# Kernel optimization log

Hardware: AMD Instinct MI355X
Metric: run time of the kernel (lower is better)

Reference implementation:

```python
import jax, jax.numpy as jnp
import numpy as np

B, N, L = 2, 2048, 2048
DQ, DKV, H, WF = 1024, 1024, 16, 4
HD = DQ // H
EPS = 1e-5


def _ln(x, g, b):
    m = jnp.mean(x, axis=-1, keepdims=True)
    v = jnp.mean(jnp.square(x - m), axis=-1, keepdims=True)
    return (x - m) * jax.lax.rsqrt(v + EPS) * g + b


def setup_inputs() -> dict:
    key = jax.random.key(0)
    ks = jax.random.split(key, 12)
    s = 0.02
    return {
        "x_q": jax.random.normal(ks[0], (B, N, DQ), jnp.float32),
        "x_kv": jax.random.normal(ks[1], (B, L, DKV), jnp.float32),
        "qn_g": jnp.ones((DQ,), jnp.float32),
        "qn_b": jnp.zeros((DQ,), jnp.float32),
        "kvn_g": jnp.ones((DKV,), jnp.float32),
        "kvn_b": jnp.zeros((DKV,), jnp.float32),
        "Wq": jax.random.normal(ks[2], (DQ, DQ), jnp.float32) * s,
        "bq": jnp.zeros((DQ,), jnp.float32),
        "Wk": jax.random.normal(ks[3], (DQ, DKV), jnp.float32) * s,
        "bk": jnp.zeros((DQ,), jnp.float32),
        "Wv": jax.random.normal(ks[4], (DQ, DKV), jnp.float32) * s,
        "bv": jnp.zeros((DQ,), jnp.float32),
        "Wo": jax.random.normal(ks[5], (DQ, DQ), jnp.float32) * s,
        "bo": jnp.zeros((DQ,), jnp.float32),
        "n2_g": jnp.ones((DQ,), jnp.float32),
        "n2_b": jnp.zeros((DQ,), jnp.float32),
        "W1": jax.random.normal(ks[6], (WF * DQ, DQ), jnp.float32) * s,
        "b1": jnp.zeros((WF * DQ,), jnp.float32),
        "W2": jax.random.normal(ks[7], (DQ, WF * DQ), jnp.float32) * s,
        "b2": jnp.zeros((DQ,), jnp.float32),
    }


def reference(x_q, x_kv, qn_g, qn_b, kvn_g, kvn_b, Wq, bq, Wk, bk, Wv, bv,
              Wo, bo, n2_g, n2_b, W1, b1, W2, b2):
    # projections (torch Linear: x @ W.T + b)
    q = (_ln(x_q, qn_g, qn_b) @ Wq.T + bq).reshape(B, N, H, HD)
    kvn = _ln(x_kv, kvn_g, kvn_b)
    k = (kvn @ Wk.T + bk).reshape(B, L, H, HD)
    v = (kvn @ Wv.T + bv).reshape(B, L, H, HD)

    # attention with softmax-1: exp(s)/(1 + sum exp(s)), numerically stable
    scale = 1.0 / jnp.sqrt(jnp.float32(HD))
    s = jnp.einsum("bnhd,blhd->bhnl", q, k) * scale  # [B,H,N,L]
    m = jnp.max(s, axis=-1, keepdims=True)
    m = jnp.maximum(m, 0.0)  # include the implicit zero logit of softmax-1
    p = jnp.exp(s - m)
    denom = jnp.sum(p, axis=-1, keepdims=True) + jnp.exp(-m)
    attn = p / denom
    attn_out = jnp.einsum("bhnl,blhd->bnhd", attn, v).reshape(B, N, DQ)

    # residual + out proj
    x = x_q + (attn_out @ Wo.T + bo)
    # residual MLP (GELU, exact/erf as torch nn.GELU default)
    h = jax.nn.gelu(_ln(x, n2_g, n2_b) @ W1.T + b1, approximate=False)
    x = x + (h @ W2.T + b2)
    return x
```

## Files before the change

kernel.cpp:

```cpp
#include <hip/hip_runtime.h>
#include <hip/hip_bf16.h>
#include <stdint.h>

#define DEV __device__ __forceinline__

typedef unsigned short ushort_t;
typedef __attribute__((ext_vector_type(8))) short bf16x8;
typedef __attribute__((ext_vector_type(4))) float f32x4;

DEV uint32_t f2bf2(float lo, float hi) {
  uint32_t d;
  asm("v_cvt_pk_bf16_f32 %0, %1, %2" : "=v"(d) : "v"(lo), "v"(hi));
  return d;
}
DEV ushort_t f2bf(float f) { return (ushort_t)f2bf2(f, f); }

DEV void gload_lds16(const void* gp, void* lp) {
  __builtin_amdgcn_global_load_lds(
      (__attribute__((address_space(1))) void*)(void*)(uintptr_t)gp,
      (__attribute__((address_space(3))) void*)lp, 16, 0, 0);
}

DEV float gelu_fast(float x) {
  const float z = fabsf(x) * 0.70710678118654752f;
  const float t = __builtin_amdgcn_rcpf(fmaf(0.3275911f, z, 1.0f));
  float p = fmaf(1.061405429f, t, -1.453152027f);
  p = fmaf(p, t, 1.421413741f);
  p = fmaf(p, t, -0.284496736f);
  p = fmaf(p, t, 0.254829592f);
  p *= t;
  const float e = __builtin_amdgcn_exp2f(z * z * -1.4426950408889634f);
  const float er = fmaf(-p, e, 1.0f);
  const float s = copysignf(er, x);
  return 0.5f * x * (1.0f + s);
}

DEV void ln_row(const float* __restrict__ x, const float* __restrict__ g,
                const float* __restrict__ be, ushort_t* __restrict__ out, int row) {
  const int t = threadIdx.x;
  const float4 v = ((const float4*)(x + (size_t)row * 1024))[t];
  float s = v.x + v.y + v.z + v.w;
  float sq = v.x * v.x + v.y * v.y + v.z * v.z + v.w * v.w;
#pragma unroll
  for (int d = 1; d < 64; d <<= 1) { s += __shfl_xor(s, d); sq += __shfl_xor(sq, d); }
  __shared__ float sm[8];
  const int w = t >> 6, lane = t & 63;
  if (lane == 0) { sm[w * 2] = s; sm[w * 2 + 1] = sq; }
  __syncthreads();
  s = sm[0] + sm[2] + sm[4] + sm[6];
  sq = sm[1] + sm[3] + sm[5] + sm[7];
  const float mean = s * (1.f / 1024.f);
  const float var = sq * (1.f / 1024.f) - mean * mean;
  const float rstd = rsqrtf(var + 1e-5f);
  const float4 gv = ((const float4*)g)[t];
  const float4 bv = ((const float4*)be)[t];
  uint2 o;
  o.x = f2bf2((v.x - mean) * rstd * gv.x + bv.x, (v.y - mean) * rstd * gv.y + bv.y);
  o.y = f2bf2((v.z - mean) * rstd * gv.z + bv.z, (v.w - mean) * rstd * gv.w + bv.w);
  ((uint2*)(out + (size_t)row * 1024))[t] = o;
}

__global__ __launch_bounds__(256) void cvt_ln(
    const float* __restrict__ Wq, const float* __restrict__ Wk,
    const float* __restrict__ Wv, const float* __restrict__ Wo,
    const float* __restrict__ W1, const float* __restrict__ W2,
    ushort_t* __restrict__ WQKVB, ushort_t* __restrict__ WoB,
    ushort_t* __restrict__ W1B, ushort_t* __restrict__ W2B,
    const float* __restrict__ x_q, const float* __restrict__ x_kv,
    const float* __restrict__ qg, const float* __restrict__ qb,
    const float* __restrict__ kg, const float* __restrict__ kb,
    ushort_t* __restrict__ oq, ushort_t* __restrict__ okv) {
  if (blockIdx.x < 12288) {
    int i = blockIdx.x * 256 + threadIdx.x;
    const float* src; ushort_t* dst; int j;
    if (i < 262144)            { src = Wq; dst = WQKVB;            j = i; }
    else if (i < 524288)       { src = Wk; dst = WQKVB + 1048576;  j = i - 262144; }
    else if (i < 786432)       { src = Wv; dst = WQKVB + 2097152;  j = i - 524288; }
    else if (i < 1048576)      { src = Wo; dst = WoB;              j = i - 786432; }
    else if (i < 2097152)      { src = W1; dst = W1B;              j = i - 1048576; }
    else                       { src = W2; dst = W2B;              j = i - 2097152; }
    float4 v = ((const float4*)src)[j];
    uint2 o; o.x = f2bf2(v.x, v.y); o.y = f2bf2(v.z, v.w);
    ((uint2*)dst)[j] = o;
  } else {
    const int r = blockIdx.x - 12288;
    if (r < 4096) ln_row(x_q, qg, qb, oq, r);
    else ln_row(x_kv, kg, kb, okv, r - 4096);
  }
}

__global__ __launch_bounds__(256) void ln_bf16(const float* __restrict__ x,
                                               const float* __restrict__ g,
                                               const float* __restrict__ be,
                                               ushort_t* __restrict__ out) {
  ln_row(x, g, be, out, blockIdx.x);
}

DEV void xcd_remap(int gx, int gy, int& bx, int& by) {
  const int lin = by * gx + bx;
  const int xcd = lin & 7, s = lin >> 3;
  by = xcd * (gy >> 3) + s / gx;
  bx = s % gx;
}

enum { EPI_BF16 = 0, EPI_KV = 1, EPI_RESID = 2, EPI_GELU = 3, EPI_QKV = 4 };

template <int BM, int TN, int BK, int EPI>
__global__ __launch_bounds__(256, (BM == 64) ? 4 : 3) void gemm_bt(
    const ushort_t* __restrict__ A,
    const ushort_t* __restrict__ A2,
    const ushort_t* __restrict__ Wb,
    const float* __restrict__ bias, const float* __restrict__ bias2,
    const float* __restrict__ bias3,
    const float* __restrict__ resid,
    void* __restrict__ outp, void* __restrict__ outp2, void* __restrict__ outp3,
    int M, int N, int K, float oscale) {
  constexpr int WAVES_N = (TN == 128 || BM == 64) ? 2 : 1;
  constexpr int WAVES_M = 4 / WAVES_N;
  constexpr int NI = BM / WAVES_M / 16;
  constexpr int NJ = TN / WAVES_N / 16;
  constexpr int CH = BK / 8;
  constexpr int NA = (BM * CH) / 256;
  constexpr int NBL = (TN * CH) / 256;
  constexpr int KS = BK / 32;
  __shared__ ushort_t As[2][BM * BK];
  __shared__ ushort_t Bs[2][TN * BK];
  const int t = threadIdx.x;
  const int w = t >> 6, lane = t & 63;
  const int qd = lane >> 4, ql = lane & 15;
  int bx = blockIdx.x, by = blockIdx.y;
  xcd_remap(gridDim.x, gridDim.y, bx, by);
  const int m0 = by * BM, n0 = bx * TN;
  const int wm = (w / WAVES_N) * (BM / WAVES_M);
  const int wn = (w % WAVES_N) * (TN / WAVES_N);
  const int sw = (BK == 64) ? (ql & 7) : ((ql >> 1) & 3);

  const ushort_t* Ause = (EPI == EPI_QKV && n0 >= 1024) ? A2 : A;

  const ushort_t* pa[NA];
#pragma unroll
  for (int p = 0; p < NA; p++) {
    int n = p * 256 + t, row = n / CH, c = n % CH;
    int g = (BK == 64) ? (c ^ (row & 7)) : (c ^ ((row >> 1) & 3));
    pa[p] = Ause + (size_t)(m0 + row) * K + g * 8;
  }
  const ushort_t* pb[NBL];
#pragma unroll
  for (int p = 0; p < NBL; p++) {
    int n = p * 256 + t, row = n / CH, c = n % CH;
    int g = (BK == 64) ? (c ^ (row & 7)) : (c ^ ((row >> 1) & 3));
    pb[p] = Wb + (size_t)(n0 + row) * K + g * 8;
  }

#pragma unroll
  for (int p = 0; p < NA; p++) { gload_lds16(pa[p], &As[0][(p * 256 + t) * 8]); pa[p] += BK; }
#pragma unroll
  for (int p = 0; p < NBL; p++) { gload_lds16(pb[p], &Bs[0][(p * 256 + t) * 8]); pb[p] += BK; }
  __syncthreads();

  f32x4 acc[NI][NJ] = {};
  const int NIT = K / BK;
  int cur = 0;

  for (int it = 0; it < NIT; ++it) {
    if (it + 1 < NIT) {
#pragma unroll
      for (int p = 0; p < NA; p++) { gload_lds16(pa[p], &As[1 ^ cur][(p * 256 + t) * 8]); pa[p] += BK; }
#pragma unroll
      for (int p = 0; p < NBL; p++) { gload_lds16(pb[p], &Bs[1 ^ cur][(p * 256 + t) * 8]); pb[p] += BK; }
    }
    const ushort_t* Ac = As[cur];
    const ushort_t* Bc = Bs[cur];
#pragma unroll
    for (int ks = 0; ks < KS; ks++) {
      bf16x8 af[NI], bf[NJ];
#pragma unroll
      for (int i = 0; i < NI; i++)
        af[i] = *(const bf16x8*)&Ac[(wm + i * 16 + ql) * BK + ((ks * 4 + qd) ^ sw) * 8];
#pragma unroll
      for (int j = 0; j < NJ; j++)
        bf[j] = *(const bf16x8*)&Bc[(wn + j * 16 + ql) * BK + ((ks * 4 + qd) ^ sw) * 8];
#pragma unroll
      for (int i = 0; i < NI; i++)
#pragma unroll
        for (int j = 0; j < NJ; j++)
          acc[i][j] = __builtin_amdgcn_mfma_f32_16x16x32_bf16(af[i], bf[j], acc[i][j], 0, 0, 0);
    }
    __syncthreads();
    cur ^= 1;
  }

#pragma unroll
  for (int i = 0; i < NI; i++) {
    const int mr = m0 + wm + i * 16 + qd * 4;
#pragma unroll
    for (int j = 0; j < NJ; j++) {
      const int col = n0 + wn + j * 16 + ql;
      f32x4 v = acc[i][j];
      if constexpr (EPI == EPI_BF16) {
        const float bb = bias[col];
        ushort_t* o = (ushort_t*)outp;
#pragma unroll
        for (int r = 0; r < 4; r++) o[(size_t)(mr + r) * N + col] = f2bf((v[r] + bb) * oscale);
      } else if constexpr (EPI == EPI_QKV) {
        if (col < 1024) {
          const float bb = bias[col];
          ushort_t* o = (ushort_t*)outp;
#pragma unroll
          for (int r = 0; r < 4; r++) o[(size_t)(mr + r) * 1024 + col] = f2bf((v[r] + bb) * oscale);
        } else if (col < 2048) {
          const int c2 = col - 1024;
          const float bb = bias2[c2];
          ushort_t* o = (ushort_t*)outp2;
#pragma unroll
          for (int r = 0; r < 4; r++) o[(size_t)(mr + r) * 1024 + c2] = f2bf(v[r] + bb);
        } else {
          const int vc = col - 2048;
          const float bb = bias3[vc];
          const int h = vc >> 6, d = vc & 63;
          const int b = mr >> 11, l0 = mr & 2047;
          uint2 pk;
          pk.x = f2bf2(v[0] + bb, v[1] + bb);
          pk.y = f2bf2(v[2] + bb, v[3] + bb);
          *(uint2*)((ushort_t*)outp3 + ((((size_t)b * 16 + h) * 64 + d) * 2048 + l0)) = pk;
        }
      } else if constexpr (EPI == EPI_RESID) {
        const float bb = bias[col];
        float* o = (float*)outp;
#pragma unroll
        for (int r = 0; r < 4; r++) {
          size_t idx = (size_t)(mr + r) * N + col;
          o[idx] = resid[idx] + v[r] + bb;
        }
      } else if constexpr (EPI == EPI_GELU) {
        const float bb = bias[col];
        ushort_t* o = (ushort_t*)outp;
#pragma unroll
        for (int r = 0; r < 4; r++)
          o[(size_t)(mr + r) * N + col] = f2bf(gelu_fast(v[r] + bb));
      }
    }
  }
}

template <int EPI>
__global__ __launch_bounds__(512, 2) void gemm256v2(
    const ushort_t* __restrict__ A, const ushort_t* __restrict__ Wb,
    const float* __restrict__ bias,
    void* __restrict__ outp, int M, int N, int K, float oscale) {
  __shared__ ushort_t As[2][256 * 64];
  __shared__ ushort_t Bs[2][256 * 64];
  const int t = threadIdx.x;
  const int w = t >> 6, lane = t & 63;
  const int qd = lane >> 4, ql = lane & 15;
  const int wr = w >> 2, wc = w & 3;
  int bx = blockIdx.x, by = blockIdx.y;
  xcd_remap(gridDim.x, gridDim.y, bx, by);
  const int m0 = by * 256, n0 = bx * 256;
  const int sw = ql & 7;

  const ushort_t* pa[4];
  const ushort_t* pb[4];
#pragma unroll
  for (int p = 0; p < 4; p++) {
    const int n = p * 512 + t, row = n >> 3, c = (n & 7) ^ (row & 7);
    pa[p] = A + (size_t)(m0 + row) * K + c * 8;
    pb[p] = Wb + (size_t)(n0 + row) * K + c * 8;
  }

#pragma unroll
  for (int p = 0; p < 4; p++) { gload_lds16(pa[p], &As[0][(p * 512 + t) * 8]); pa[p] += 64; }
#pragma unroll
  for (int p = 0; p < 4; p++) { gload_lds16(pb[p], &Bs[0][(p * 512 + t) * 8]); pb[p] += 64; }
  __syncthreads();

  f32x4 acc[8][4] = {};
  const int NT = K / 64;
  int cur = 0;

#define AFREAD(KS)                                                              \
  _Pragma("unroll") for (int i = 0; i < 8; i++)                                 \
      af[i] = *(const bf16x8*)&Ac[(wr * 128 + i * 16 + ql) * 64 +               \
                                  (((KS) * 4 + qd) ^ sw) * 8];
#define BFREAD(KS, NH)                                                          \
  _Pragma("unroll") for (int jj = 0; jj < 2; jj++)                              \
      bf[jj] = *(const bf16x8*)&Bc[(wc * 64 + (NH) * 32 + jj * 16 + ql) * 64 +  \
                                   (((KS) * 4 + qd) ^ sw) * 8];
#define MM(NH)                                                                  \
  __builtin_amdgcn_s_setprio(1);                                                \
  _Pragma("unroll") for (int i = 0; i < 8; i++)                                 \
      _Pragma("unroll") for (int jj = 0; jj < 2; jj++)                          \
          acc[i][(NH) * 2 + jj] = __builtin_amdgcn_mfma_f32_16x16x32_bf16(      \
              af[i], bf[jj], acc[i][(NH) * 2 + jj], 0, 0, 0);                   \
  __builtin_amdgcn_s_setprio(0);

  for (int T = 0; T < NT; ++T) {
    const ushort_t* Ac = As[cur];
    const ushort_t* Bc = Bs[cur];
    ushort_t* An = As[cur ^ 1];
    ushort_t* Bn = Bs[cur ^ 1];
    const bool st = (T + 1 < NT);
    bf16x8 af[8], bf[2];

    if (st) {
#pragma unroll
      for (int p = 0; p < 4; p++) { gload_lds16(pa[p], &An[(p * 512 + t) * 8]); pa[p] += 64; }
#pragma unroll
      for (int p = 0; p < 4; p++) { gload_lds16(pb[p], &Bn[(p * 512 + t) * 8]); pb[p] += 64; }
    }
    AFREAD(0)
    BFREAD(0, 0)
    MM(0)
    __builtin_amdgcn_s_barrier();

    BFREAD(0, 1)
    MM(1)
    __builtin_amdgcn_s_barrier();

    AFREAD(1)
    BFREAD(1, 0)
    MM(0)
    __builtin_amdgcn_s_barrier();

    BFREAD(1, 1)
    MM(1)
    if (st) asm volatile("s_waitcnt vmcnt(0)" ::: "memory");
    __builtin_amdgcn_sched_barrier(0);
    __builtin_amdgcn_s_barrier();
    __builtin_amdgcn_sched_barrier(0);
    cur ^= 1;
  }
#undef AFREAD
#undef BFREAD
#undef MM

#pragma unroll
  for (int i = 0; i < 8; i++) {
    const int mr = m0 + wr * 128 + i * 16 + qd * 4;
#pragma unroll
    for (int j = 0; j < 4; j++) {
      const int col = n0 + wc * 64 + j * 16 + ql;
      f32x4 v = acc[i][j];
      if constexpr (EPI == EPI_GELU) {
        const float bb = bias[col];
        ushort_t* o = (ushort_t*)outp;
#pragma unroll
        for (int r = 0; r < 4; r++)
          o[(size_t)(mr + r) * N + col] = f2bf(gelu_fast(v[r] + bb));
      } else if constexpr (EPI == EPI_BF16) {
        const float bb = bias[col];
        ushort_t* o = (ushort_t*)outp;
#pragma unroll
        for (int r = 0; r < 4; r++)
          o[(size_t)(mr + r) * N + col] = f2bf((v[r] + bb) * oscale);
      }
    }
  }
}

__global__ __launch_bounds__(256, 2) void flash_attn(const ushort_t* __restrict__ Qg,
                                                     const ushort_t* __restrict__ Kg,
                                                     const ushort_t* __restrict__ VTg,
                                                     ushort_t* __restrict__ Og) {
  __shared__ ushort_t QPs[128 * 64];
  __shared__ ushort_t Ks[2][64 * 64];
  __shared__ ushort_t Vs[2][64 * 64];
  const int t = threadIdx.x, w = t >> 6, lane = t & 63;
  const int qd = lane >> 4, ql = lane & 15;
  int bx = blockIdx.x, bh = blockIdx.y;
  xcd_remap(gridDim.x, gridDim.y, bx, bh);
  const int b = bh >> 4, h = bh & 15;
  const int n0 = bx * 128;
  const ushort_t* Qp = Qg + ((size_t)b * 2048 + n0) * 1024 + h * 64;
  const ushort_t* Kp = Kg + (size_t)b * 2048 * 1024 + h * 64;
  const ushort_t* Vp = VTg + (size_t)bh * 64 * 2048;
  const int sw = ql & 7;

  const ushort_t* kp2[2];
  const ushort_t* vp2[2];
#pragma unroll
  for (int p = 0; p < 2; p++) {
    int n = p * 256 + t, row = n >> 3, c = (n & 7) ^ (row & 7);
    kp2[p] = Kp + (size_t)row * 1024 + c * 8;
    vp2[p] = Vp + (size_t)row * 2048 + c * 8;
  }

#pragma unroll
  for (int p = 0; p < 4; p++) {
    int n = p * 256 + t, row = n >> 3, c = (n & 7) ^ (row & 7);
    gload_lds16(Qp + (size_t)row * 1024 + c * 8, &QPs[n * 8]);
  }
#pragma unroll
  for (int p = 0; p < 2; p++) {
    int n = p * 256 + t;
    gload_lds16(kp2[p], &Ks[0][n * 8]);
    gload_lds16(vp2[p], &Vs[0][n * 8]);
    kp2[p] += 64 * 1024;
    vp2[p] += 64;
  }
  __syncthreads();

  bf16x8 aq[2][2];
#pragma unroll
  for (int i = 0; i < 2; i++)
#pragma unroll
    for (int ks = 0; ks < 2; ks++)
      aq[i][ks] = *(const bf16x8*)&QPs[(w * 32 + i * 16 + ql) * 64 + ((ks * 4 + qd) ^ sw) * 8];
  __syncthreads();

  f32x4 accO[2][4] = {};
  float lro2[2] = {0.f, 0.f};

  int cur = 0;
  for (int lt = 0; lt < 32; ++lt) {
    if (lt + 1 < 32) {
#pragma unroll
      for (int p = 0; p < 2; p++) {
        int n = p * 256 + t;
        gload_lds16(kp2[p], &Ks[1 ^ cur][n * 8]);
        gload_lds16(vp2[p], &Vs[1 ^ cur][n * 8]);
        kp2[p] += 64 * 1024;
        vp2[p] += 64;
      }
    }
    const ushort_t* Kc = Ks[cur];
    const ushort_t* Vc = Vs[cur];

    f32x4 accS[4][2] = {};
#pragma unroll
    for (int ks = 0; ks < 2; ks++) {
      bf16x8 bk[4];
#pragma unroll
      for (int j = 0; j < 4; j++)
        bk[j] = *(const bf16x8*)&Kc[(j * 16 + ql) * 64 + ((ks * 4 + qd) ^ sw) * 8];
      __builtin_amdgcn_s_setprio(1);
#pragma unroll
      for (int j = 0; j < 4; j++)
#pragma unroll
        for (int i = 0; i < 2; i++)
          accS[j][i] = __builtin_amdgcn_mfma_f32_16x16x32_bf16(bk[j], aq[i][ks], accS[j][i], 0, 0, 0);
      __builtin_amdgcn_s_setprio(0);
    }

#pragma unroll
    for (int j = 0; j < 4; j++)
#pragma unroll
      for (int i = 0; i < 2; i++) {
        f32x4 p;
#pragma unroll
        for (int r = 0; r < 4; r++) {
          p[r] = __builtin_amdgcn_exp2f(accS[j][i][r]);
          lro2[i] += p[r];
        }
        const int n = w * 32 + i * 16 + ql;
        const int coff = (((j * 2 + (qd >> 1)) ^ sw) << 3) + ((qd & 1) << 2);
        uint2 pk; pk.x = f2bf2(p[0], p[1]); pk.y = f2bf2(p[2], p[3]);
        *(uint2*)&QPs[n * 64 + coff] = pk;
      }

#pragma unroll
    for (int ks = 0; ks < 2; ks++) {
      bf16x8 ap[2], bv[4];
#pragma unroll
      for (int i = 0; i < 2; i++)
        ap[i] = *(const bf16x8*)&QPs[(w * 32 + i * 16 + ql) * 64 + ((ks * 4 + qd) ^ sw) * 8];
#pragma unroll
      for (int jo = 0; jo < 4; jo++)
        bv[jo] = *(const bf16x8*)&Vc[(jo * 16 + ql) * 64 + ((ks * 4 + qd) ^ sw) * 8];
      __builtin_amdgcn_s_setprio(1);
#pragma unroll
      for (int i = 0; i < 2; i++)
#pragma unroll
        for (int jo = 0; jo < 4; jo++)
          accO[i][jo] = __builtin_amdgcn_mfma_f32_16x16x32_bf16(ap[i], bv[jo], accO[i][jo], 0, 0, 0);
      __builtin_amdgcn_s_setprio(0);
    }

    __syncthreads();
    cur ^= 1;
  }

  float dn[2];
#pragma unroll
  for (int i = 0; i < 2; i++) {
    float l = lro2[i];
    l += __shfl_xor(l, 16);
    l += __shfl_xor(l, 32);
    dn[i] = l + 1.0f;
  }

#pragma unroll
  for (int i = 0; i < 2; i++)
#pragma unroll
    for (int r = 0; r < 4; r++) {
      const float inv = 1.0f / __shfl(dn[i], qd * 4 + r);
      const int row = n0 + w * 32 + i * 16 + qd * 4 + r;
#pragma unroll
      for (int jo = 0; jo < 4; jo++)
        Og[((size_t)b * 2048 + row) * 1024 + h * 64 + jo * 16 + ql] =
            f2bf(accO[i][jo][r] * inv);
    }
}

extern "C" void kernel_launch(void* const* d_in, const int* in_sizes, int n_in,
                              void* d_out, int out_size, void* d_ws, size_t ws_size,
                              hipStream_t stream) {
  const float* x_q = (const float*)d_in[0];
  const float* x_kv = (const float*)d_in[1];
  const float* qn_g = (const float*)d_in[2];
  const float* qn_b = (const float*)d_in[3];
  const float* kvn_g = (const float*)d_in[4];
  const float* kvn_b = (const float*)d_in[5];
  const float* Wq = (const float*)d_in[6];
  const float* bq = (const float*)d_in[7];
  const float* Wk = (const float*)d_in[8];
  const float* bk = (const float*)d_in[9];
  const float* Wv = (const float*)d_in[10];
  const float* bv = (const float*)d_in[11];
  const float* Wo = (const float*)d_in[12];
  const float* bo = (const float*)d_in[13];
  const float* n2_g = (const float*)d_in[14];
  const float* n2_b = (const float*)d_in[15];
  const float* W1 = (const float*)d_in[16];
  const float* b1 = (const float*)d_in[17];
  const float* W2 = (const float*)d_in[18];
  const float* b2 = (const float*)d_in[19];

  char* ws = (char*)d_ws;
  const size_t MB = 1ull << 20;
  ushort_t* WQKVB = (ushort_t*)(ws + 0 * MB);
  ushort_t* WoB = (ushort_t*)(ws + 6 * MB);
  ushort_t* W1B = (ushort_t*)(ws + 8 * MB);
  ushort_t* W2B = (ushort_t*)(ws + 16 * MB);
  ushort_t* LNQ = (ushort_t*)(ws + 24 * MB);
  ushort_t* LNKV = (ushort_t*)(ws + 32 * MB);
  ushort_t* Qb = (ushort_t*)(ws + 40 * MB);
  ushort_t* Kb = (ushort_t*)(ws + 48 * MB);
  ushort_t* VTb = (ushort_t*)(ws + 56 * MB);
  ushort_t* AOb = (ushort_t*)(ws + 64 * MB);
  float* Xf = (float*)(ws + 72 * MB);
  ushort_t* LN2 = (ushort_t*)(ws + 88 * MB);
  ushort_t* Hb = (ushort_t*)(ws + 24 * MB);

  const float QSCALE = 0.18033688011112042f;

  cvt_ln<<<20480, 256, 0, stream>>>(Wq, Wk, Wv, Wo, W1, W2, WQKVB, WoB, W1B, W2B,
                                    x_q, x_kv, qn_g, qn_b, kvn_g, kvn_b, LNQ, LNKV);

  gemm_bt<128, 128, 32, EPI_QKV><<<dim3(24, 32), 256, 0, stream>>>(
      LNQ, LNKV, WQKVB, bq, bk, bv, nullptr, Qb, Kb, VTb, 4096, 3072, 1024, QSCALE);

  flash_attn<<<dim3(16, 32), 256, 0, stream>>>(Qb, Kb, VTb, AOb);

  gemm_bt<64, 64, 64, EPI_RESID><<<dim3(16, 64), 256, 0, stream>>>(
      AOb, nullptr, WoB, bo, nullptr, nullptr, x_q, Xf, nullptr, nullptr,
      4096, 1024, 1024, 1.0f);
  ln_bf16<<<4096, 256, 0, stream>>>(Xf, n2_g, n2_b, LN2);
  gemm256v2<EPI_GELU><<<dim3(16, 16), 512, 0, stream>>>(
      LN2, W1B, b1, Hb, 4096, 4096, 1024, 1.0f);
  gemm_bt<64, 64, 64, EPI_RESID><<<dim3(16, 64), 256, 0, stream>>>(
      Hb, nullptr, W2B, b2, nullptr, nullptr, Xf, (float*)d_out, nullptr, nullptr,
      4096, 1024, 4096, 1.0f);
}
```

Before: 354.3 us.

## Software-pipeline attention loop so next tile's QK overlaps current softmax and PV

Restructures the flash-attention main loop into a two-stage software pipeline. K is staged one tile ahead of V, and the QK^T MFMAs for tile t+1 are issued before the exp2/softmax and PV MFMAs of tile t, using alternating accumulators accA and accB. The aim is to fill the MFMA units during the transcendental and LDS write phases and to hide load latency. The cost is more live accumulator registers, which may lower occupancy, plus a more complex macro-unrolled prologue and epilogue.

```diff
diff --git a/kernel.cpp b/kernel.cpp
--- a/kernel.cpp
+++ b/kernel.cpp
@@ -391,13 +391,7 @@
     gload_lds16(Qp + (size_t)row * 1024 + c * 8, &QPs[n * 8]);
   }
 #pragma unroll
-  for (int p = 0; p < 2; p++) {
-    int n = p * 256 + t;
-    gload_lds16(kp2[p], &Ks[0][n * 8]);
-    gload_lds16(vp2[p], &Vs[0][n * 8]);
-    kp2[p] += 64 * 1024;
-    vp2[p] += 64;
-  }
+  for (int p = 0; p < 2; p++) { gload_lds16(kp2[p], &Ks[0][(p * 256 + t) * 8]); kp2[p] += 64 * 1024; }
   __syncthreads();
 
   bf16x8 aq[2][2];
@@ -408,77 +402,101 @@
       aq[i][ks] = *(const bf16x8*)&QPs[(w * 32 + i * 16 + ql) * 64 + ((ks * 4 + qd) ^ sw) * 8];
   __syncthreads();
 
+  f32x4 accA[4][2], accB[4][2];
   f32x4 accO[2][4] = {};
   float lro2[2] = {0.f, 0.f};
-
-  int cur = 0;
-  for (int lt = 0; lt < 32; ++lt) {
-    if (lt + 1 < 32) {
-#pragma unroll
-      for (int p = 0; p < 2; p++) {
-        int n = p * 256 + t;
-        gload_lds16(kp2[p], &Ks[1 ^ cur][n * 8]);
-        gload_lds16(vp2[p], &Vs[1 ^ cur][n * 8]);
-        kp2[p] += 64 * 1024;
-        vp2[p] += 64;
-      }
-    }
-    const ushort_t* Kc = Ks[cur];
-    const ushort_t* Vc = Vs[cur];
-
-    f32x4 accS[4][2] = {};
-#pragma unroll
-    for (int ks = 0; ks < 2; ks++) {
-      bf16x8 bk[4];
-#pragma unroll
-      for (int j = 0; j < 4; j++)
-        bk[j] = *(const bf16x8*)&Kc[(j * 16 + ql) * 64 + ((ks * 4 + qd) ^ sw) * 8];
-      __builtin_amdgcn_s_setprio(1);
-#pragma unroll
-      for (int j = 0; j < 4; j++)
-#pragma unroll
-        for (int i = 0; i < 2; i++)
-          accS[j][i] = __builtin_amdgcn_mfma_f32_16x16x32_bf16(bk[j], aq[i][ks], accS[j][i], 0, 0, 0);
-      __builtin_amdgcn_s_setprio(0);
-    }
-
-#pragma unroll
-    for (int j = 0; j < 4; j++)
-#pragma unroll
-      for (int i = 0; i < 2; i++) {
-        f32x4 p;
-#pragma unroll
-        for (int r = 0; r < 4; r++) {
-          p[r] = __builtin_amdgcn_exp2f(accS[j][i][r]);
-          lro2[i] += p[r];
-        }
-        const int n = w * 32 + i * 16 + ql;
-        const int coff = (((j * 2 + (qd >> 1)) ^ sw) << 3) + ((qd & 1) << 2);
-        uint2 pk; pk.x = f2bf2(p[0], p[1]); pk.y = f2bf2(p[2], p[3]);
-        *(uint2*)&QPs[n * 64 + coff] = pk;
-      }
-
-#pragma unroll
-    for (int ks = 0; ks < 2; ks++) {
-      bf16x8 ap[2], bv[4];
-#pragma unroll
-      for (int i = 0; i < 2; i++)
-        ap[i] = *(const bf16x8*)&QPs[(w * 32 + i * 16 + ql) * 64 + ((ks * 4 + qd) ^ sw) * 8];
-#pragma unroll
-      for (int jo = 0; jo < 4; jo++)
-        bv[jo] = *(const bf16x8*)&Vc[(jo * 16 + ql) * 64 + ((ks * 4 + qd) ^ sw) * 8];
-      __builtin_amdgcn_s_setprio(1);
-#pragma unroll
-      for (int i = 0; i < 2; i++)
-#pragma unroll
-        for (int jo = 0; jo < 4; jo++)
-          accO[i][jo] = __builtin_amdgcn_mfma_f32_16x16x32_bf16(ap[i], bv[jo], accO[i][jo], 0, 0, 0);
-      __builtin_amdgcn_s_setprio(0);
-    }
-
+  const f32x4 ZZ = {0.f, 0.f, 0.f, 0.f};
+
+#define QKSTEP(ACC, KSLOT)                                                                \
+  { const ushort_t* Kc_ = &Ks[KSLOT][0];                                                  \
+    bf16x8 bk[4];                                                                         \
+    _Pragma("unroll") for (int j = 0; j < 4; j++)                                         \
+      bk[j] = *(const bf16x8*)&Kc_[(j * 16 + ql) * 64 + ((0 + qd) ^ sw) * 8];             \
+    __builtin_amdgcn_s_setprio(1);                                                        \
+    _Pragma("unroll") for (int j = 0; j < 4; j++)                                         \
+      _Pragma("unroll") for (int i = 0; i < 2; i++)                                       \
+        ACC[j][i] = __builtin_amdgcn_mfma_f32_16x16x32_bf16(bk[j], aq[i][0], ZZ, 0, 0, 0);\
+    __builtin_amdgcn_s_setprio(0);                                                        \
+    _Pragma("unroll") for (int j = 0; j < 4; j++)                                         \
+      bk[j] = *(const bf16x8*)&Kc_[(j * 16 + ql) * 64 + ((4 + qd) ^ sw) * 8];             \
+    __builtin_amdgcn_s_setprio(1);                                                        \
+    _Pragma("unroll") for (int j = 0; j < 4; j++)                                         \
+      _Pragma("unroll") for (int i = 0; i < 2; i++)                                       \
+        ACC[j][i] = __builtin_amdgcn_mfma_f32_16x16x32_bf16(bk[j], aq[i][1], ACC[j][i], 0, 0, 0); \
+    __builtin_amdgcn_s_setprio(0);                                                        \
+  }
+
+#define SMSTEP(ACC)                                                                       \
+  _Pragma("unroll") for (int j = 0; j < 4; j++)                                           \
+    _Pragma("unroll") for (int i = 0; i < 2; i++) {                                       \
+      f32x4 pp;                                                                           \
+      _Pragma("unroll") for (int r = 0; r < 4; r++) {                                     \
+        pp[r] = __builtin_amdgcn_exp2f(ACC[j][i][r]);                                     \
+        lro2[i] += pp[r];                                                                 \
+      }                                                                                   \
+      const int nn = w * 32 + i * 16 + ql;                                                \
+      const int coff = (((j * 2 + (qd >> 1)) ^ sw) << 3) + ((qd & 1) << 2);               \
+      uint2 pk_; pk_.x = f2bf2(pp[0], pp[1]); pk_.y = f2bf2(pp[2], pp[3]);                \
+      *(uint2*)&QPs[nn * 64 + coff] = pk_;                                                \
+    }
+
+#define PVSTEP(VSLOT)                                                                     \
+  { const ushort_t* Vc_ = &Vs[VSLOT][0];                                                  \
+    _Pragma("unroll") for (int ks = 0; ks < 2; ks++) {                                    \
+      bf16x8 ap[2], bv[4];                                                                \
+      _Pragma("unroll") for (int i = 0; i < 2; i++)                                       \
+        ap[i] = *(const bf16x8*)&QPs[(w * 32 + i * 16 + ql) * 64 + ((ks * 4 + qd) ^ sw) * 8]; \
+      _Pragma("unroll") for (int jo = 0; jo < 4; jo++)                                    \
+        bv[jo] = *(const bf16x8*)&Vc_[(jo * 16 + ql) * 64 + ((ks * 4 + qd) ^ sw) * 8];    \
+      __builtin_amdgcn_s_setprio(1);                                                      \
+      _Pragma("unroll") for (int i = 0; i < 2; i++)                                       \
+        _Pragma("unroll") for (int jo = 0; jo < 4; jo++)                                  \
+          accO[i][jo] = __builtin_amdgcn_mfma_f32_16x16x32_bf16(ap[i], bv[jo], accO[i][jo], 0, 0, 0); \
+      __builtin_amdgcn_s_setprio(0);                                                      \
+    }                                                                                     \
+  }
+
+#define STAGE_K(SLOT)                                                                     \
+  _Pragma("unroll") for (int q_ = 0; q_ < 2; q_++) {                                      \
+    gload_lds16(kp2[q_], &Ks[SLOT][(q_ * 256 + t) * 8]); kp2[q_] += 64 * 1024;            \
+  }
+#define STAGE_V(SLOT)                                                                     \
+  _Pragma("unroll") for (int q_ = 0; q_ < 2; q_++) {                                      \
+    gload_lds16(vp2[q_], &Vs[SLOT][(q_ * 256 + t) * 8]); vp2[q_] += 64;                   \
+  }
+
+  STAGE_K(1)
+  STAGE_V(0)
+  QKSTEP(accA, 0)
+  __syncthreads();
+
+  for (int tt = 1; tt < 31; tt += 2) {
+    STAGE_K(0)
+    STAGE_V(1)
+    QKSTEP(accB, 1)
+    SMSTEP(accA)
+    PVSTEP(0)
     __syncthreads();
-    cur ^= 1;
-  }
+    STAGE_K(1)
+    STAGE_V(0)
+    QKSTEP(accA, 0)
+    SMSTEP(accB)
+    PVSTEP(1)
+    __syncthreads();
+  }
+  STAGE_V(1)
+  QKSTEP(accB, 1)
+  SMSTEP(accA)
+  PVSTEP(0)
+  __syncthreads();
+  SMSTEP(accB)
+  PVSTEP(1)
+
+#undef QKSTEP
+#undef SMSTEP
+#undef PVSTEP
+#undef STAGE_K
+#undef STAGE_V
 
   float dn[2];
 #pragma unroll
```

Result: no change. 350.9 us (median of 2 runs) (-0.9%).
